# Optimization experiments

Hardware: AMD Instinct MI355X
Metric: run time of the kernel (lower is better)

Reference implementation:

```python
import jax, jax.numpy as jnp
import numpy as np

B, T, H = 32, 4096, 512


def setup_inputs() -> dict:
    key = jax.random.key(0)
    k1, k2, k3, k4, k5 = jax.random.split(key, 5)
    stdv = 1.0 / np.sqrt(2 * H)
    stdv_v = 1.0 / np.sqrt(H)
    return {
        "hidden": jax.random.normal(k1, (B, H), dtype=jnp.float32),
        "encoder_outputs": jax.random.normal(k2, (T, B, H), dtype=jnp.float32),
        "W_attn": jax.random.uniform(k3, (H, 2 * H), minval=-stdv, maxval=stdv, dtype=jnp.float32),
        "b_attn": jax.random.uniform(k4, (H,), minval=-stdv, maxval=stdv, dtype=jnp.float32),
        "v": jax.random.uniform(k5, (H,), minval=-stdv_v, maxval=stdv_v, dtype=jnp.float32),
    }


def reference(hidden, encoder_outputs, W_attn, b_attn, v):
    # hidden: [B, H]; encoder_outputs: [T, B, H]
    T_ = encoder_outputs.shape[0]
    h = jnp.broadcast_to(hidden[None, :, :], (T_,) + hidden.shape).transpose(1, 0, 2)  # [B,T,H]
    enc = encoder_outputs.transpose(1, 0, 2)  # [B,T,H]
    cat = jnp.concatenate([h, enc], axis=2)  # [B,T,2H]
    # Linear(2H -> H) then legacy F.softmax with implicit dim=0 for 3D input (batch axis)
    energy = jax.nn.softmax(jnp.einsum('btk,hk->bth', cat, W_attn) + b_attn, axis=0)  # [B,T,H]
    # bmm(v[B,1,H], energy^T[B,H,T]) -> [B,1,T] -> squeeze -> [B,T]
    scores = jnp.einsum('h,bth->bt', v, energy)
    return jax.nn.relu(scores)[:, None, :]  # [B,1,T]
```

## Files before the change

kernel.cpp:

```cpp
#include <hip/hip_runtime.h>
#include <hip/hip_bf16.h>

#define B_ 32
#define T_ 4096
#define H_ 512
#define TILE_T 4
#define M_TILE 128
#define BK 64
#define KSTEPS 8
#define NTHREADS 512

typedef __attribute__((ext_vector_type(8))) short short8;
typedef __attribute__((ext_vector_type(8))) __bf16 bf16x8;
typedef __attribute__((ext_vector_type(4))) float f32x4;

__device__ __forceinline__ short f2bf(float f) {
    unsigned u = __builtin_bit_cast(unsigned, f);
    u = (u + 0x7fffu + ((u >> 16) & 1u)) >> 16;
    return (short)u;
}

__global__ void prep_w2(const float* __restrict__ W, short* __restrict__ w2p) {
    int idx = blockIdx.x * 256 + threadIdx.x;
    int kp = idx & 63;
    int h  = (idx >> 6) & 511;
    int s  = idx >> 15;
    int k  = s * BK + (((kp >> 3) ^ (h & 7)) << 3) + (kp & 7);
    w2p[idx] = f2bf(W[h * (2 * H_) + H_ + k]);
}

__global__ void prep_hid(const float* __restrict__ hidden,
                         const float* __restrict__ W,
                         const float* __restrict__ bias,
                         float* __restrict__ hidproj) {
    __shared__ float hrow[H_];
    int b = blockIdx.y;
    int h = blockIdx.x * 128 + threadIdx.x;
    for (int i = threadIdx.x; i < H_; i += 128) hrow[i] = hidden[b * H_ + i];
    __syncthreads();
    const float* wr = W + (size_t)h * (2 * H_);
    float acc = bias[h];
#pragma unroll 4
    for (int k = 0; k < H_; k += 4) {
        acc += hrow[k]     * wr[k];
        acc += hrow[k + 1] * wr[k + 1];
        acc += hrow[k + 2] * wr[k + 2];
        acc += hrow[k + 3] * wr[k + 3];
    }
    hidproj[b * H_ + h] = acc;
}

__global__ __launch_bounds__(NTHREADS, 2)
void attn_main(const float* __restrict__ enc,
               const float* __restrict__ hidproj,
               const short* __restrict__ w2p,
               const float* __restrict__ vvec,
               float* __restrict__ out)
{
    __shared__ __align__(16) short lds_w[2][H_ * BK];
    __shared__ __align__(16) short lds_a[2][M_TILE * BK];

    const int tid  = threadIdx.x;
    const int lane = tid & 63;
    const int wid  = tid >> 6;
    const int t0   = blockIdx.x * TILE_T;
    const int n0   = wid * 64;
    const int lo   = lane & 15;
    const int hi4  = lane >> 4;

    f32x4 acc[8][4];
#pragma unroll
    for (int i = 0; i < 8; ++i)
#pragma unroll
        for (int j = 0; j < 4; ++j) acc[i][j] = f32x4{0.f, 0.f, 0.f, 0.f};

    const int arow = tid >> 2;
    const int akc  = tid & 3;
    const float* abase = enc + (size_t)(t0 * B_ + arow) * H_ + akc * 16;

    {
        const float* s = abase;
        f32x4 x0 = *(const f32x4*)(s);
        f32x4 x1 = *(const f32x4*)(s + 4);
        f32x4 x2 = *(const f32x4*)(s + 8);
        f32x4 x3 = *(const f32x4*)(s + 12);
#pragma unroll
        for (int r = 0; r < 8; ++r) {
            __builtin_amdgcn_global_load_lds(
                (const __attribute__((address_space(1))) void*)(w2p + r * 4096 + tid * 8),
                (__attribute__((address_space(3))) void*)(&lds_w[0][r * 4096 + wid * 512]),
                16, 0, 0);
        }
        short8 p0, p1;
        p0[0]=f2bf(x0[0]); p0[1]=f2bf(x0[1]); p0[2]=f2bf(x0[2]); p0[3]=f2bf(x0[3]);
        p0[4]=f2bf(x1[0]); p0[5]=f2bf(x1[1]); p0[6]=f2bf(x1[2]); p0[7]=f2bf(x1[3]);
        p1[0]=f2bf(x2[0]); p1[1]=f2bf(x2[1]); p1[2]=f2bf(x2[2]); p1[3]=f2bf(x2[3]);
        p1[4]=f2bf(x3[0]); p1[5]=f2bf(x3[1]); p1[6]=f2bf(x3[2]); p1[7]=f2bf(x3[3]);
        *(short8*)&lds_a[0][arow * BK + (((2 * akc)     ^ (arow & 7)) << 3)] = p0;
        *(short8*)&lds_a[0][arow * BK + (((2 * akc + 1) ^ (arow & 7)) << 3)] = p1;
        __syncthreads();
    }

#define PHASE_MFMA(AF, BF, MIBASE)                                              \
    __builtin_amdgcn_s_barrier();                                               \
    asm volatile("s_waitcnt lgkmcnt(0)" ::: "memory");                          \
    __builtin_amdgcn_sched_barrier(0);                                          \
    __builtin_amdgcn_s_setprio(1);                                              \
    _Pragma("unroll")                                                           \
    for (int mi = 0; mi < 4; ++mi)                                              \
        _Pragma("unroll")                                                       \
        for (int ni = 0; ni < 4; ++ni)                                          \
            acc[(MIBASE) + mi][ni] = __builtin_amdgcn_mfma_f32_16x16x32_bf16(   \
                AF[mi], BF[ni], acc[(MIBASE) + mi][ni], 0, 0, 0);               \
    __builtin_amdgcn_s_setprio(0);                                              \
    __builtin_amdgcn_sched_barrier(0);

    for (int kk = 0; kk < KSTEPS; ++kk) {
        const int cur = kk & 1;
        const int nx  = kk + 1;
        const bool pf = nx < KSTEPS;
        const short* __restrict__ wb = &lds_w[cur][0];
        const short* __restrict__ ab = &lds_a[cur][0];
        short* __restrict__ wdst = &lds_w[cur ^ 1][0];
        short* __restrict__ adst = &lds_a[cur ^ 1][0];
        const short* wsrc = w2p + (size_t)nx * (H_ * BK);
        const float* asrc = abase + (size_t)nx * BK;

        f32x4 x0, x1, x2, x3;
        bf16x8 b0[4], b1[4], af[4];

#pragma unroll
        for (int ni = 0; ni < 4; ++ni) {
            int r = n0 + ni * 16 + lo;
            b0[ni] = *(const bf16x8*)&wb[r * BK + (((hi4) ^ (r & 7)) << 3)];
        }
#pragma unroll
        for (int mi = 0; mi < 4; ++mi) {
            int r = mi * 16 + lo;
            af[mi] = *(const bf16x8*)&ab[r * BK + (((hi4) ^ (r & 7)) << 3)];
        }
        if (pf) {
            x0 = *(const f32x4*)(asrc);
            x1 = *(const f32x4*)(asrc + 4);
#pragma unroll
            for (int r = 0; r < 2; ++r)
                __builtin_amdgcn_global_load_lds(
                    (const __attribute__((address_space(1))) void*)(wsrc + r * 4096 + tid * 8),
                    (__attribute__((address_space(3))) void*)(wdst + r * 4096 + wid * 512),
                    16, 0, 0);
        }
        PHASE_MFMA(af, b0, 0)
        __builtin_amdgcn_s_barrier();

#pragma unroll
        for (int mi = 0; mi < 4; ++mi) {
            int r = (mi + 4) * 16 + lo;
            af[mi] = *(const bf16x8*)&ab[r * BK + (((hi4) ^ (r & 7)) << 3)];
        }
        if (pf) {
            x2 = *(const f32x4*)(asrc + 8);
            x3 = *(const f32x4*)(asrc + 12);
#pragma unroll
            for (int r = 2; r < 4; ++r)
                __builtin_amdgcn_global_load_lds(
                    (const __attribute__((address_space(1))) void*)(wsrc + r * 4096 + tid * 8),
                    (__attribute__((address_space(3))) void*)(wdst + r * 4096 + wid * 512),
                    16, 0, 0);
        }
        PHASE_MFMA(af, b0, 4)
        __builtin_amdgcn_s_barrier();

#pragma unroll
        for (int ni = 0; ni < 4; ++ni) {
            int r = n0 + ni * 16 + lo;
            b1[ni] = *(const bf16x8*)&wb[r * BK + (((4 | hi4) ^ (r & 7)) << 3)];
        }
#pragma unroll
        for (int mi = 0; mi < 4; ++mi) {
            int r = mi * 16 + lo;
            af[mi] = *(const bf16x8*)&ab[r * BK + (((4 | hi4) ^ (r & 7)) << 3)];
        }
        if (pf) {
#pragma unroll
            for (int r = 4; r < 6; ++r)
                __builtin_amdgcn_global_load_lds(
                    (const __attribute__((address_space(1))) void*)(wsrc + r * 4096 + tid * 8),
                    (__attribute__((address_space(3))) void*)(wdst + r * 4096 + wid * 512),
                    16, 0, 0);
            short8 p0;
            p0[0]=f2bf(x0[0]); p0[1]=f2bf(x0[1]); p0[2]=f2bf(x0[2]); p0[3]=f2bf(x0[3]);
            p0[4]=f2bf(x1[0]); p0[5]=f2bf(x1[1]); p0[6]=f2bf(x1[2]); p0[7]=f2bf(x1[3]);
            *(short8*)&adst[arow * BK + (((2 * akc) ^ (arow & 7)) << 3)] = p0;
        }
        PHASE_MFMA(af, b1, 0)
        __builtin_amdgcn_s_barrier();

#pragma unroll
        for (int mi = 0; mi < 4; ++mi) {
            int r = (mi + 4) * 16 + lo;
            af[mi] = *(const bf16x8*)&ab[r * BK + (((4 | hi4) ^ (r & 7)) << 3)];
        }
        if (pf) {
#pragma unroll
            for (int r = 6; r < 8; ++r)
                __builtin_amdgcn_global_load_lds(
                    (const __attribute__((address_space(1))) void*)(wsrc + r * 4096 + tid * 8),
                    (__attribute__((address_space(3))) void*)(wdst + r * 4096 + wid * 512),
                    16, 0, 0);
            short8 p1;
            p1[0]=f2bf(x2[0]); p1[1]=f2bf(x2[1]); p1[2]=f2bf(x2[2]); p1[3]=f2bf(x2[3]);
            p1[4]=f2bf(x3[0]); p1[5]=f2bf(x3[1]); p1[6]=f2bf(x3[2]); p1[7]=f2bf(x3[3]);
            *(short8*)&adst[arow * BK + (((2 * akc + 1) ^ (arow & 7)) << 3)] = p1;
        }
        PHASE_MFMA(af, b1, 4)
        if (pf) {
            asm volatile("s_waitcnt vmcnt(0)" ::: "memory");
            __builtin_amdgcn_sched_barrier(0);
        }
        __builtin_amdgcn_s_barrier();
    }
#undef PHASE_MFMA

    {
        float hp[2][4][4];
#pragma unroll
        for (int par = 0; par < 2; ++par)
#pragma unroll
            for (int j = 0; j < 4; ++j) {
                int b = par * 16 + hi4 * 4 + j;
#pragma unroll
                for (int ni = 0; ni < 4; ++ni)
                    hp[par][j][ni] = hidproj[b * H_ + n0 + ni * 16 + lo];
            }
#pragma unroll
        for (int mi = 0; mi < 8; ++mi)
#pragma unroll
            for (int ni = 0; ni < 4; ++ni)
#pragma unroll
                for (int j = 0; j < 4; ++j)
                    acc[mi][ni][j] += hp[mi & 1][j][ni];
    }

    float vh[4];
#pragma unroll
    for (int ni = 0; ni < 4; ++ni) vh[ni] = vvec[n0 + ni * 16 + lo];

    float scp[8][4];
#pragma unroll
    for (int tl = 0; tl < 4; ++tl) {
        const int m0 = tl * 2, m1 = tl * 2 + 1;
#pragma unroll
        for (int ni = 0; ni < 4; ++ni) {
            float mx = -1e30f;
#pragma unroll
            for (int j = 0; j < 4; ++j) {
                mx = fmaxf(mx, acc[m0][ni][j]);
                mx = fmaxf(mx, acc[m1][ni][j]);
            }
            mx = fmaxf(mx, __shfl_xor(mx, 16));
            mx = fmaxf(mx, __shfl_xor(mx, 32));
            float e0[4], e1[4];
            float sum = 0.f;
#pragma unroll
            for (int j = 0; j < 4; ++j) {
                e0[j] = __expf(acc[m0][ni][j] - mx);
                e1[j] = __expf(acc[m1][ni][j] - mx);
                sum += e0[j] + e1[j];
            }
            sum += __shfl_xor(sum, 16);
            sum += __shfl_xor(sum, 32);
            float rs = vh[ni] / sum;
#pragma unroll
            for (int j = 0; j < 4; ++j) {
                if (ni == 0) { scp[m0][j] = e0[j] * rs; scp[m1][j] = e1[j] * rs; }
                else         { scp[m0][j] += e0[j] * rs; scp[m1][j] += e1[j] * rs; }
            }
        }
    }

#pragma unroll
    for (int mi = 0; mi < 8; ++mi)
#pragma unroll
        for (int j = 0; j < 4; ++j) {
            float x = scp[mi][j];
            x += __shfl_xor(x, 1);
            x += __shfl_xor(x, 2);
            x += __shfl_xor(x, 4);
            x += __shfl_xor(x, 8);
            scp[mi][j] = x;
        }

    __syncthreads();
    float* red = (float*)&lds_a[0][0];
    if (lo == 0) {
#pragma unroll
        for (int mi = 0; mi < 8; ++mi)
#pragma unroll
            for (int j = 0; j < 4; ++j)
                red[wid * 128 + mi * 16 + hi4 * 4 + j] = scp[mi][j];
    }
    __syncthreads();
    if (tid < 128) {
        float s = 0.f;
#pragma unroll
        for (int w = 0; w < 8; ++w) s += red[w * 128 + tid];
        int b  = tid & 31;
        int tl = tid >> 5;
        out[(size_t)b * T_ + (t0 + tl)] = fmaxf(s, 0.f);
    }
}

extern "C" void kernel_launch(void* const* d_in, const int* in_sizes, int n_in,
                              void* d_out, int out_size, void* d_ws, size_t ws_size,
                              hipStream_t stream) {
    const float* hidden = (const float*)d_in[0];
    const float* enc    = (const float*)d_in[1];
    const float* W      = (const float*)d_in[2];
    const float* bias   = (const float*)d_in[3];
    const float* v      = (const float*)d_in[4];
    float* out = (float*)d_out;

    float* hidproj = (float*)d_ws;
    short* w2p     = (short*)((char*)d_ws + 65536);

    prep_w2<<<1024, 256, 0, stream>>>(W, w2p);
    prep_hid<<<dim3(4, 32), 128, 0, stream>>>(hidden, W, bias, hidproj);
    attn_main<<<T_ / TILE_T, NTHREADS, 0, stream>>>(enc, hidproj, w2p, v, out);
}
```

Before: 140.8 us.

## Load pre-swizzled W fragments directly from global into registers, dropping W LDS staging

The weight matrix is now pre-packed into MFMA fragment order so each wave loads its B operands straight from global memory (L2-resident) into registers, removing the W double-buffer in LDS and its global_load_lds traffic. The per-phase barriers are also collapsed into one barrier per K step. This cuts LDS footprint from 160KB to 32KB per block and cuts synchronisation. The cost is that B fragments are exposed to global latency with no prefetch ahead of the MFMAs, which may stall waves.

New measurement: 128.6 us. 8.7% less time.

```diff
diff --git a/kernel.cpp b/kernel.cpp
--- a/kernel.cpp
+++ b/kernel.cpp
@@ -20,13 +20,17 @@
     return (short)u;
 }
 
-__global__ void prep_w2(const float* __restrict__ W, short* __restrict__ w2p) {
+__global__ void prep_w2f(const float* __restrict__ W, short* __restrict__ w2f) {
     int idx = blockIdx.x * 256 + threadIdx.x;
-    int kp = idx & 63;
-    int h  = (idx >> 6) & 511;
-    int s  = idx >> 15;
-    int k  = s * BK + (((kp >> 3) ^ (h & 7)) << 3) + (kp & 7);
-    w2p[idx] = f2bf(W[h * (2 * H_) + H_ + k]);
+    int j    = idx & 7;
+    int lane = (idx >> 3) & 63;
+    int ni   = (idx >> 9) & 3;
+    int ks   = (idx >> 11) & 1;
+    int kk   = (idx >> 12) & 7;
+    int c    = (idx >> 15) & 7;
+    int h = c * 64 + ni * 16 + (lane & 15);
+    int k = kk * 64 + ks * 32 + (lane >> 4) * 8 + j;
+    w2f[idx] = f2bf(W[h * (2 * H_) + H_ + k]);
 }
 
 __global__ void prep_hid(const float* __restrict__ hidden,
@@ -53,11 +57,10 @@
 __global__ __launch_bounds__(NTHREADS, 2)
 void attn_main(const float* __restrict__ enc,
                const float* __restrict__ hidproj,
-               const short* __restrict__ w2p,
+               const short* __restrict__ w2f,
                const float* __restrict__ vvec,
                float* __restrict__ out)
 {
-    __shared__ __align__(16) short lds_w[2][H_ * BK];
     __shared__ __align__(16) short lds_a[2][M_TILE * BK];
 
     const int tid  = threadIdx.x;
@@ -74,152 +77,130 @@
 #pragma unroll
         for (int j = 0; j < 4; ++j) acc[i][j] = f32x4{0.f, 0.f, 0.f, 0.f};
 
+    const short* wbase = w2f + (size_t)wid * 32768 + lane * 8;
+
     const int arow = tid >> 2;
     const int akc  = tid & 3;
     const float* abase = enc + (size_t)(t0 * B_ + arow) * H_ + akc * 16;
+    const int aw0 = arow * BK + (((2 * akc)     ^ (arow & 7)) << 3);
+    const int aw1 = arow * BK + (((2 * akc + 1) ^ (arow & 7)) << 3);
 
     {
-        const float* s = abase;
-        f32x4 x0 = *(const f32x4*)(s);
-        f32x4 x1 = *(const f32x4*)(s + 4);
-        f32x4 x2 = *(const f32x4*)(s + 8);
-        f32x4 x3 = *(const f32x4*)(s + 12);
-#pragma unroll
-        for (int r = 0; r < 8; ++r) {
-            __builtin_amdgcn_global_load_lds(
-                (const __attribute__((address_space(1))) void*)(w2p + r * 4096 + tid * 8),
-                (__attribute__((address_space(3))) void*)(&lds_w[0][r * 4096 + wid * 512]),
-                16, 0, 0);
-        }
+        f32x4 x0 = *(const f32x4*)(abase);
+        f32x4 x1 = *(const f32x4*)(abase + 4);
+        f32x4 x2 = *(const f32x4*)(abase + 8);
+        f32x4 x3 = *(const f32x4*)(abase + 12);
         short8 p0, p1;
         p0[0]=f2bf(x0[0]); p0[1]=f2bf(x0[1]); p0[2]=f2bf(x0[2]); p0[3]=f2bf(x0[3]);
         p0[4]=f2bf(x1[0]); p0[5]=f2bf(x1[1]); p0[6]=f2bf(x1[2]); p0[7]=f2bf(x1[3]);
         p1[0]=f2bf(x2[0]); p1[1]=f2bf(x2[1]); p1[2]=f2bf(x2[2]); p1[3]=f2bf(x2[3]);
         p1[4]=f2bf(x3[0]); p1[5]=f2bf(x3[1]); p1[6]=f2bf(x3[2]); p1[7]=f2bf(x3[3]);
-        *(short8*)&lds_a[0][arow * BK + (((2 * akc)     ^ (arow & 7)) << 3)] = p0;
-        *(short8*)&lds_a[0][arow * BK + (((2 * akc + 1) ^ (arow & 7)) << 3)] = p1;
-        __syncthreads();
-    }
-
-#define PHASE_MFMA(AF, BF, MIBASE)                                              \
-    __builtin_amdgcn_s_barrier();                                               \
-    asm volatile("s_waitcnt lgkmcnt(0)" ::: "memory");                          \
-    __builtin_amdgcn_sched_barrier(0);                                          \
-    __builtin_amdgcn_s_setprio(1);                                              \
-    _Pragma("unroll")                                                           \
-    for (int mi = 0; mi < 4; ++mi)                                              \
-        _Pragma("unroll")                                                       \
-        for (int ni = 0; ni < 4; ++ni)                                          \
-            acc[(MIBASE) + mi][ni] = __builtin_amdgcn_mfma_f32_16x16x32_bf16(   \
-                AF[mi], BF[ni], acc[(MIBASE) + mi][ni], 0, 0, 0);               \
-    __builtin_amdgcn_s_setprio(0);                                              \
-    __builtin_amdgcn_sched_barrier(0);
+        *(short8*)&lds_a[0][aw0] = p0;
+        *(short8*)&lds_a[0][aw1] = p1;
+        asm volatile("s_waitcnt lgkmcnt(0)" ::: "memory");
+        __builtin_amdgcn_s_barrier();
+    }
 
     for (int kk = 0; kk < KSTEPS; ++kk) {
         const int cur = kk & 1;
-        const int nx  = kk + 1;
-        const bool pf = nx < KSTEPS;
-        const short* __restrict__ wb = &lds_w[cur][0];
+        const bool pf = (kk + 1) < KSTEPS;
         const short* __restrict__ ab = &lds_a[cur][0];
-        short* __restrict__ wdst = &lds_w[cur ^ 1][0];
         short* __restrict__ adst = &lds_a[cur ^ 1][0];
-        const short* wsrc = w2p + (size_t)nx * (H_ * BK);
-        const float* asrc = abase + (size_t)nx * BK;
+
+        bf16x8 b0[4], b1[4];
+#pragma unroll
+        for (int ni = 0; ni < 4; ++ni)
+            b0[ni] = *(const bf16x8*)(wbase + ((kk * 2 + 0) * 4 + ni) * 512);
+#pragma unroll
+        for (int ni = 0; ni < 4; ++ni)
+            b1[ni] = *(const bf16x8*)(wbase + ((kk * 2 + 1) * 4 + ni) * 512);
 
         f32x4 x0, x1, x2, x3;
-        bf16x8 b0[4], b1[4], af[4];
-
-#pragma unroll
-        for (int ni = 0; ni < 4; ++ni) {
-            int r = n0 + ni * 16 + lo;
-            b0[ni] = *(const bf16x8*)&wb[r * BK + (((hi4) ^ (r & 7)) << 3)];
-        }
-#pragma unroll
-        for (int mi = 0; mi < 4; ++mi) {
-            int r = mi * 16 + lo;
-            af[mi] = *(const bf16x8*)&ab[r * BK + (((hi4) ^ (r & 7)) << 3)];
-        }
         if (pf) {
+            const float* asrc = abase + (size_t)(kk + 1) * BK;
             x0 = *(const f32x4*)(asrc);
             x1 = *(const f32x4*)(asrc + 4);
-#pragma unroll
-            for (int r = 0; r < 2; ++r)
-                __builtin_amdgcn_global_load_lds(
-                    (const __attribute__((address_space(1))) void*)(wsrc + r * 4096 + tid * 8),
-                    (__attribute__((address_space(3))) void*)(wdst + r * 4096 + wid * 512),
-                    16, 0, 0);
-        }
-        PHASE_MFMA(af, b0, 0)
-        __builtin_amdgcn_s_barrier();
-
-#pragma unroll
-        for (int mi = 0; mi < 4; ++mi) {
-            int r = (mi + 4) * 16 + lo;
-            af[mi] = *(const bf16x8*)&ab[r * BK + (((hi4) ^ (r & 7)) << 3)];
-        }
-        if (pf) {
             x2 = *(const f32x4*)(asrc + 8);
             x3 = *(const f32x4*)(asrc + 12);
-#pragma unroll
-            for (int r = 2; r < 4; ++r)
-                __builtin_amdgcn_global_load_lds(
-                    (const __attribute__((address_space(1))) void*)(wsrc + r * 4096 + tid * 8),
-                    (__attribute__((address_space(3))) void*)(wdst + r * 4096 + wid * 512),
-                    16, 0, 0);
-        }
-        PHASE_MFMA(af, b0, 4)
-        __builtin_amdgcn_s_barrier();
-
-#pragma unroll
-        for (int ni = 0; ni < 4; ++ni) {
-            int r = n0 + ni * 16 + lo;
-            b1[ni] = *(const bf16x8*)&wb[r * BK + (((4 | hi4) ^ (r & 7)) << 3)];
-        }
-#pragma unroll
-        for (int mi = 0; mi < 4; ++mi) {
-            int r = mi * 16 + lo;
-            af[mi] = *(const bf16x8*)&ab[r * BK + (((4 | hi4) ^ (r & 7)) << 3)];
-        }
+        }
+
+        {
+            bf16x8 af[4];
+#pragma unroll
+            for (int mi = 0; mi < 4; ++mi) {
+                int r = mi * 16 + lo;
+                af[mi] = *(const bf16x8*)&ab[r * BK + ((hi4 ^ (r & 7)) << 3)];
+            }
+            __builtin_amdgcn_s_setprio(1);
+#pragma unroll
+            for (int mi = 0; mi < 4; ++mi)
+#pragma unroll
+                for (int ni = 0; ni < 4; ++ni)
+                    acc[mi][ni] = __builtin_amdgcn_mfma_f32_16x16x32_bf16(
+                        af[mi], b0[ni], acc[mi][ni], 0, 0, 0);
+            __builtin_amdgcn_s_setprio(0);
+#pragma unroll
+            for (int mi = 0; mi < 4; ++mi) {
+                int r = (mi + 4) * 16 + lo;
+                af[mi] = *(const bf16x8*)&ab[r * BK + ((hi4 ^ (r & 7)) << 3)];
+            }
+            __builtin_amdgcn_s_setprio(1);
+#pragma unroll
+            for (int mi = 0; mi < 4; ++mi)
+#pragma unroll
+                for (int ni = 0; ni < 4; ++ni)
+                    acc[mi + 4][ni] = __builtin_amdgcn_mfma_f32_16x16x32_bf16(
+                        af[mi], b0[ni], acc[mi + 4][ni], 0, 0, 0);
+            __builtin_amdgcn_s_setprio(0);
+        }
+
         if (pf) {
-#pragma unroll
-            for (int r = 4; r < 6; ++r)
-                __builtin_amdgcn_global_load_lds(
-                    (const __attribute__((address_space(1))) void*)(wsrc + r * 4096 + tid * 8),
-                    (__attribute__((address_space(3))) void*)(wdst + r * 4096 + wid * 512),
-                    16, 0, 0);
             short8 p0;
             p0[0]=f2bf(x0[0]); p0[1]=f2bf(x0[1]); p0[2]=f2bf(x0[2]); p0[3]=f2bf(x0[3]);
             p0[4]=f2bf(x1[0]); p0[5]=f2bf(x1[1]); p0[6]=f2bf(x1[2]); p0[7]=f2bf(x1[3]);
-            *(short8*)&adst[arow * BK + (((2 * akc) ^ (arow & 7)) << 3)] = p0;
-        }
-        PHASE_MFMA(af, b1, 0)
-        __builtin_amdgcn_s_barrier();
-
-#pragma unroll
-        for (int mi = 0; mi < 4; ++mi) {
-            int r = (mi + 4) * 16 + lo;
-            af[mi] = *(const bf16x8*)&ab[r * BK + (((4 | hi4) ^ (r & 7)) << 3)];
-        }
+            *(short8*)&adst[aw0] = p0;
+        }
+
+        {
+            bf16x8 af[4];
+#pragma unroll
+            for (int mi = 0; mi < 4; ++mi) {
+                int r = mi * 16 + lo;
+                af[mi] = *(const bf16x8*)&ab[r * BK + (((4 | hi4) ^ (r & 7)) << 3)];
+            }
+            __builtin_amdgcn_s_setprio(1);
+#pragma unroll
+            for (int mi = 0; mi < 4; ++mi)
+#pragma unroll
+                for (int ni = 0; ni < 4; ++ni)
+                    acc[mi][ni] = __builtin_amdgcn_mfma_f32_16x16x32_bf16(
+                        af[mi], b1[ni], acc[mi][ni], 0, 0, 0);
+            __builtin_amdgcn_s_setprio(0);
+#pragma unroll
+            for (int mi = 0; mi < 4; ++mi) {
+                int r = (mi + 4) * 16 + lo;
+                af[mi] = *(const bf16x8*)&ab[r * BK + (((4 | hi4) ^ (r & 7)) << 3)];
+            }
+            __builtin_amdgcn_s_setprio(1);
+#pragma unroll
+            for (int mi = 0; mi < 4; ++mi)
+#pragma unroll
+                for (int ni = 0; ni < 4; ++ni)
+                    acc[mi + 4][ni] = __builtin_amdgcn_mfma_f32_16x16x32_bf16(
+                        af[mi], b1[ni], acc[mi + 4][ni], 0, 0, 0);
+            __builtin_amdgcn_s_setprio(0);
+        }
+
         if (pf) {
-#pragma unroll
-            for (int r = 6; r < 8; ++r)
-                __builtin_amdgcn_global_load_lds(
-                    (const __attribute__((address_space(1))) void*)(wsrc + r * 4096 + tid * 8),
-                    (__attribute__((address_space(3))) void*)(wdst + r * 4096 + wid * 512),
-                    16, 0, 0);
             short8 p1;
             p1[0]=f2bf(x2[0]); p1[1]=f2bf(x2[1]); p1[2]=f2bf(x2[2]); p1[3]=f2bf(x2[3]);
             p1[4]=f2bf(x3[0]); p1[5]=f2bf(x3[1]); p1[6]=f2bf(x3[2]); p1[7]=f2bf(x3[3]);
-            *(short8*)&adst[arow * BK + (((2 * akc + 1) ^ (arow & 7)) << 3)] = p1;
-        }
-        PHASE_MFMA(af, b1, 4)
-        if (pf) {
-            asm volatile("s_waitcnt vmcnt(0)" ::: "memory");
-            __builtin_amdgcn_sched_barrier(0);
-        }
+            *(short8*)&adst[aw1] = p1;
+        }
+
+        asm volatile("s_waitcnt lgkmcnt(0)" ::: "memory");
         __builtin_amdgcn_s_barrier();
     }
-#undef PHASE_MFMA
 
     {
         float hp[2][4][4];
@@ -321,9 +302,9 @@
     float* out = (float*)d_out;
 
     float* hidproj = (float*)d_ws;
-    short* w2p     = (short*)((char*)d_ws + 65536);
-
-    prep_w2<<<1024, 256, 0, stream>>>(W, w2p);
+    short* w2f     = (short*)((char*)d_ws + 65536);
+
+    prep_w2f<<<1024, 256, 0, stream>>>(W, w2f);
     prep_hid<<<dim3(4, 32), 128, 0, stream>>>(hidden, W, bias, hidproj);
-    attn_main<<<T_ / TILE_T, NTHREADS, 0, stream>>>(enc, hidproj, w2p, v, out);
-}
+    attn_main<<<T_ / TILE_T, NTHREADS, 0, stream>>>(enc, hidproj, w2f, v, out);
+}
```
